# Performance work log

Hardware: AMD Instinct MI355X
Metric: run time of the kernel (lower is better)

## Reference

```python
import jax, jax.numpy as jnp
import numpy as np

N = 50000      # nodes
E = 800000     # edges
IN = 128       # in_dim
OUT = 128      # out_dim
R = 4          # num_relations
H = 8          # heads
D = OUT // H   # per-head dim
NEG_SLOPE = 0.2


def setup_inputs() -> dict:
    key = jax.random.key(0)
    ks = jax.random.split(key, 12)
    s = 0.05
    return {
        "node_inp": jax.random.normal(ks[0], (N, IN), dtype=jnp.float32),
        "edge_index": jax.random.randint(ks[1], (2, E), 0, N),
        "edge_type": jax.random.randint(ks[2], (E,), 0, R),
        # per-relation GATConv params
        "W_rel": jax.random.normal(ks[3], (R, IN, OUT), dtype=jnp.float32) * s,
        "att_src_rel": jax.random.normal(ks[4], (R, H, D), dtype=jnp.float32) * s,
        "att_dst_rel": jax.random.normal(ks[5], (R, H, D), dtype=jnp.float32) * s,
        "bias_rel": jax.random.normal(ks[6], (R, OUT), dtype=jnp.float32) * s,
        # linear layers
        "W_self": jax.random.normal(ks[7], (IN, OUT), dtype=jnp.float32) * s,   # lin_self
        "W_cross": jax.random.normal(ks[8], (OUT, OUT), dtype=jnp.float32) * s,  # lin_cross
        # lang_conv GAT params (lin_l is Bypass, so no weight matrix)
        "att_src_lang": jax.random.normal(ks[9], (H, D), dtype=jnp.float32) * s,
        "att_dst_lang": jax.random.normal(ks[10], (H, D), dtype=jnp.float32) * s,
        "bias_lang": jax.random.normal(ks[11], (OUT,), dtype=jnp.float32) * s,
    }


def _hgnn_forward(node_inp, edge_index, edge_type, W_rel, att_src_rel,
                  att_dst_rel, bias_rel, W_self, W_cross,
                  att_src_lang, att_dst_lang, bias_lang):
    src, dst = edge_index[0], edge_index[1]

    def rel_gat(W, a_s, a_d, b, mask):
        # standard PyG GATConv (single x, add_self_loops=False), restricted to
        # edges with this relation type via mask
        x = (node_inp @ W).reshape(N, H, D)                     # [N,H,D]
        es = jnp.einsum('nhd,hd->nh', x, a_s)
        ed = jnp.einsum('nhd,hd->nh', x, a_d)
        logit = jax.nn.leaky_relu(es[src] + ed[dst], NEG_SLOPE)  # [E,H]
        logit = jnp.where(mask[:, None], logit, -1e30)
        mx = jax.ops.segment_max(logit, dst, num_segments=N)     # [N,H]
        mx = jnp.maximum(mx, -1e30)                              # avoid -inf
        p = jnp.exp(logit - mx[dst]) * mask[:, None]
        den = jax.ops.segment_sum(p, dst, num_segments=N)        # [N,H]
        alpha = p / jnp.where(den > 0, den, 1.0)[dst]            # [E,H]
        msg = alpha[..., None] * x[src]                          # [E,H,D]
        out = jax.ops.segment_sum(msg, dst, num_segments=N)      # [N,H,D]
        tmask = jax.ops.segment_sum(mask.astype(jnp.float32), dst,
                                    num_segments=N) > 0          # [N] target nodes
        return out.reshape(N, OUT) + b, tmask

    rel_masks = edge_type[None, :] == jnp.arange(R)[:, None]     # [R,E]
    rel_out, tmask = jax.vmap(rel_gat)(W_rel, att_src_rel, att_dst_rel,
                                       bias_rel, rel_masks)      # [R,N,OUT],[R,N]
    h = jax.nn.gelu(rel_out, approximate=False) @ W_cross        # [R,N,OUT]

    S = node_inp @ W_self                                        # [N,OUT] self entries
    # lang_conv: per node i, GAT attention over entries {self(i)} U
    # {rel outputs at i for relations where i is a target}. lin_l = Bypass,
    # and since x is a single tensor in PyG, x_dst = rel_inputs[i] = S[i].
    ent = jnp.concatenate([S[None], h], axis=0).reshape(R + 1, N, H, D)
    valid = jnp.concatenate([jnp.ones((1, N), bool), tmask], axis=0)  # [R+1,N]
    ls = jnp.einsum('knhd,hd->knh', ent, att_src_lang)
    ld = jnp.einsum('nhd,hd->nh', ent[0], att_dst_lang)
    logit = jax.nn.leaky_relu(ls + ld[None], NEG_SLOPE)          # [R+1,N,H]
    logit = jnp.where(valid[..., None], logit, -jnp.inf)
    alpha = jax.nn.softmax(logit, axis=0)                        # self always valid
    out = jnp.einsum('knh,knhd->nhd', alpha, ent).reshape(N, OUT)
    return out + bias_lang


def reference(node_inp, edge_index, edge_type, W_rel, att_src_rel, att_dst_rel,
              bias_rel, W_self, W_cross, att_src_lang, att_dst_lang, bias_lang):
    return _hgnn_forward(node_inp, edge_index, edge_type, W_rel, att_src_rel,
                         att_dst_rel, bias_rel, W_self, W_cross,
                         att_src_lang, att_dst_lang, bias_lang)
```

## Files before the change

kernel.cpp:

```cpp
#include <hip/hip_runtime.h>
#include <hip/hip_bf16.h>
#include <math.h>

#define NN 50000
#define NE 800000
#define NREL 4
#define NHEAD 8
#define NSEG (NREL * NN)
#define BCAP 26

typedef __hip_bfloat16 bf16;
typedef short short8 __attribute__((ext_vector_type(8)));
typedef float floatx4 __attribute__((ext_vector_type(4)));

#define LOG2E 1.4426950408889634f

__device__ __forceinline__ float b2f(bf16 v) { return __bfloat162float(v); }
__device__ __forceinline__ float us2f(unsigned short u) {
    return __uint_as_float(((unsigned)u) << 16);
}
__device__ __forceinline__ unsigned short f2us(float v) {
    bf16 b = __float2bfloat16(v);
    return *(unsigned short*)&b;
}

__device__ __forceinline__ float gelu_f(float v) {
    float z = v * 0.70710678118654752f;
    float az = fabsf(z);
    float t = __builtin_amdgcn_rcpf(__builtin_fmaf(0.3275911f, az, 1.f));
    float p = t * (0.254829592f +
              t * (-0.284496736f +
              t * (1.421413741f +
              t * (-1.453152027f +
              t * 1.061405429f))));
    float ex = __builtin_amdgcn_exp2f(az * az * -LOG2E);
    float er = copysignf(1.f - p * ex, z);
    return 0.5f * v * (1.f + er);
}

__global__ void fill_kernel(float* __restrict__ out, int n) {
    int t = blockIdx.x * blockDim.x + threadIdx.x;
    if (t < n) out[t] = 1000.0f;
}

__global__ __launch_bounds__(256) void prep_scatter(
    const float* __restrict__ W_rel,
    const float* __restrict__ W_self,
    const float* __restrict__ W_cross,
    const float* __restrict__ a_src,
    const float* __restrict__ a_dst,
    const float* __restrict__ node_inp,
    const int* __restrict__ ei,
    const int* __restrict__ et,
    bf16* __restrict__ Wt, bf16* __restrict__ Wct,
    bf16* __restrict__ Ab,
    int* __restrict__ counts,
    unsigned short* __restrict__ bkt) {
    int t = blockIdx.x * blockDim.x + threadIdx.x;

    int src = 0, pos = BCAP;
    unsigned seg = 0;
    if (t < NE) {
        src = ei[t];
        int dst = ei[NE + t];
        seg = (unsigned)(et[t] * NN + dst);
        pos = atomicAdd(&counts[seg], 1);
    }

    if (t < 768 * 128) {
        int row = t >> 7, k = t & 127;
        float v;
        if (row < 512) {
            int r = row >> 7, c = row & 127;
            v = W_rel[(r * 128 + k) * 128 + c];
        } else if (row < 640) {
            v = W_self[k * 128 + (row - 512)];
        } else if (row < 704) {
            int q = row - 640;
            bool is_src = q < 32;
            int qq = is_src ? q : q - 32;
            int r = qq >> 3, h = qq & 7;
            const float* av = (is_src ? a_src : a_dst) + (r * 8 + h) * 16;
            const float* wr = W_rel + (size_t)(r * 128 + k) * 128 + h * 16;
            float s = 0.f;
            #pragma unroll
            for (int dd = 0; dd < 16; ++dd) s += wr[dd] * av[dd];
            v = s * LOG2E;
        } else {
            v = 0.f;
        }
        Wt[t] = __float2bfloat16(v);
    } else if (t < 768 * 128 + 128 * 128) {
        int u = t - 768 * 128;
        int n = u >> 7, k = u & 127;
        Wct[u] = __float2bfloat16(W_cross[k * 128 + n]);
    }

    if (t < NN * 16) {
        const float* ap = node_inp + (size_t)t * 8;
        float4 f0 = *(const float4*)ap;
        float4 f1 = *(const float4*)(ap + 4);
        short8 v = (short8){(short)f2us(f0.x), (short)f2us(f0.y),
                            (short)f2us(f0.z), (short)f2us(f0.w),
                            (short)f2us(f1.x), (short)f2us(f1.y),
                            (short)f2us(f1.z), (short)f2us(f1.w)};
        *(short8*)(Ab + (size_t)t * 8) = v;
    }

    if (t < NE && pos < BCAP)
        bkt[seg * (unsigned)BCAP + (unsigned)pos] = (unsigned short)src;
}

__global__ __launch_bounds__(256) void gemm_node(
    const bf16* __restrict__ Ab,
    const bf16* __restrict__ Bt,
    bf16* __restrict__ outb,
    float* __restrict__ outf,
    unsigned short* __restrict__ es_u,
    unsigned short* __restrict__ ed_u,
    int M)
{
    __shared__ __align__(16) char smem[25600];
    short (*As)[40] = (short (*)[40])smem;
    short (*Bs)[40] = (short (*)[40])(smem + 5120);

    const int tid  = threadIdx.x;
    const int wave = tid >> 6, lane = tid & 63;
    const int quad = lane >> 4, l16 = lane & 15;
    const int wr_ = wave & 1, wc = wave >> 1;
    const int row0 = blockIdx.x * 64;
    const int plane = blockIdx.y;
    const int col0 = plane * 256;

    floatx4 acc[2][8];
    #pragma unroll
    for (int i = 0; i < 2; ++i)
        #pragma unroll
        for (int j = 0; j < 8; ++j) acc[i][j] = (floatx4){0.f, 0.f, 0.f, 0.f};

    for (int k0 = 0; k0 < 128; k0 += 32) {
        {
            int c = tid;
            int r = c >> 2, off = (c & 3) * 8;
            int gr = row0 + r;
            short8 v = {0, 0, 0, 0, 0, 0, 0, 0};
            if (gr < M)
                v = *(const short8*)(Ab + (((size_t)gr) << 7) + k0 + off);
            *(short8*)&As[r][off] = v;
        }
        #pragma unroll
        for (int i = 0; i < 4; ++i) {
            int c = i * 256 + tid;
            int r = c >> 2, off = (c & 3) * 8;
            short8 w = *(const short8*)(Bt + (((size_t)(col0 + r)) << 7) + k0 + off);
            *(short8*)&Bs[r][off] = w;
        }
        __syncthreads();

        short8 av[2], bv[8];
        #pragma unroll
        for (int mt = 0; mt < 2; ++mt)
            av[mt] = *(const short8*)&As[wr_ * 32 + mt * 16 + l16][quad * 8];
        #pragma unroll
        for (int nt = 0; nt < 8; ++nt)
            bv[nt] = *(const short8*)&Bs[wc * 128 + nt * 16 + l16][quad * 8];
        #pragma unroll
        for (int mt = 0; mt < 2; ++mt)
            #pragma unroll
            for (int nt = 0; nt < 8; ++nt)
                acc[mt][nt] = __builtin_amdgcn_mfma_f32_16x16x32_bf16(
                    av[mt], bv[nt], acc[mt][nt], 0, 0, 0);
        __syncthreads();
    }

    const bool eswave = (plane == 2 && wc == 1);
    if (eswave) {
        #pragma unroll
        for (int mt = 0; mt < 2; ++mt) {
            #pragma unroll
            for (int reg = 0; reg < 4; ++reg) {
                int gr = row0 + wr_ * 32 + mt * 16 + quad * 4 + reg;
                if (gr >= M) continue;
                #pragma unroll
                for (int nt = 0; nt < 4; ++nt) {
                    int q = nt * 16 + l16;
                    unsigned short v = f2us(acc[mt][nt][reg]);
                    if (q < 32)
                        es_u[(unsigned)((q >> 3) * NN + gr) * 8u + (unsigned)(q & 7)] = v;
                    else
                        ed_u[(unsigned)(((q - 32) >> 3) * NN + gr) * 8u + (unsigned)((q - 32) & 7)] = v;
                }
            }
        }
    }

    float* ct = (float*)(smem + wave * 4352);
    const int rr2 = lane >> 2;
    const int cc0 = (lane & 3) * 16;

    for (int mt = 0; mt < 2; ++mt) {
        #pragma unroll
        for (int half = 0; half < 2; ++half) {
            if (!eswave) {
                #pragma unroll
                for (int nt = 0; nt < 4; ++nt)
                    #pragma unroll
                    for (int reg = 0; reg < 4; ++reg)
                        ct[(quad * 4 + reg) * 68 + nt * 16 + l16] =
                            acc[mt][half * 4 + nt][reg];
            }
            __syncthreads();
            if (!eswave) {
                int gr2 = row0 + wr_ * 32 + mt * 16 + rr2;
                if (gr2 < M) {
                    float4 f0 = *(const float4*)&ct[rr2 * 68 + cc0];
                    float4 f1 = *(const float4*)&ct[rr2 * 68 + cc0 + 4];
                    float4 f2 = *(const float4*)&ct[rr2 * 68 + cc0 + 8];
                    float4 f3 = *(const float4*)&ct[rr2 * 68 + cc0 + 12];
                    int lc = half * 64 + cc0;
                    if (plane == 2) {
                        float* dst = outf + (((size_t)gr2) << 7) + lc;
                        ((float4*)dst)[0] = f0;
                        ((float4*)dst)[1] = f1;
                        ((float4*)dst)[2] = f2;
                        ((float4*)dst)[3] = f3;
                    } else {
                        int rel = plane * 2 + wc;
                        float tmp[16] = {f0.x, f0.y, f0.z, f0.w, f1.x, f1.y, f1.z, f1.w,
                                         f2.x, f2.y, f2.z, f2.w, f3.x, f3.y, f3.z, f3.w};
                        short8 o0, o1;
                        #pragma unroll
                        for (int j = 0; j < 8; ++j) o0[j] = (short)f2us(tmp[j]);
                        #pragma unroll
                        for (int j = 0; j < 8; ++j) o1[j] = (short)f2us(tmp[8 + j]);
                        bf16* dst = outb + ((size_t)(rel * NN + gr2) << 7) + lc;
                        *(short8*)dst = o0;
                        *(short8*)(dst + 8) = o1;
                    }
                }
            }
            __syncthreads();
        }
    }
}

__global__ __launch_bounds__(256) void agg_kernel(
    const unsigned short* __restrict__ bkt, const int* __restrict__ counts,
    const bf16* __restrict__ Xb, const unsigned short* __restrict__ es_u,
    const unsigned short* __restrict__ ed_u, const float* __restrict__ bias_rel,
    bf16* __restrict__ Gb4, unsigned char* __restrict__ flag)
{
    const int rel = blockIdx.y;
    const int n = blockIdx.x * 4 + (threadIdx.x >> 6);
    if (n >= NN) return;
    const int l = threadIdx.x & 63;
    const int h = l >> 3;
    const int f = l * 2;
    const unsigned seg = (unsigned)(rel * NN + n);
    int cnt = __builtin_amdgcn_readfirstlane(counts[seg]);
    cnt = cnt < BCAP ? cnt : BCAP;
    const unsigned short* bk = bkt + seg * (unsigned)BCAP;
    const float edv = us2f(ed_u[seg * 8u + (unsigned)h]);
    float a0 = 0.f, a1 = 0.f, den = 0.f;
    const unsigned short* Xr = (const unsigned short*)Xb + (unsigned)rel * (unsigned)(NN * 128);
    const unsigned short* esr = es_u + (unsigned)rel * (unsigned)(NN * 8);

    int e = 0;
    for (; e + 3 < cnt; e += 4) {
        int s0 = __builtin_amdgcn_readfirstlane((int)bk[e]);
        int s1 = __builtin_amdgcn_readfirstlane((int)bk[e + 1]);
        int s2 = __builtin_amdgcn_readfirstlane((int)bk[e + 2]);
        int s3 = __builtin_amdgcn_readfirstlane((int)bk[e + 3]);
        float e0 = us2f(esr[(unsigned)s0 * 8u + (unsigned)h]);
        float e1 = us2f(esr[(unsigned)s1 * 8u + (unsigned)h]);
        float e2 = us2f(esr[(unsigned)s2 * 8u + (unsigned)h]);
        float e3 = us2f(esr[(unsigned)s3 * 8u + (unsigned)h]);
        ushort2 u0 = *(const ushort2*)(Xr + (unsigned)s0 * 128u + (unsigned)f);
        ushort2 u1 = *(const ushort2*)(Xr + (unsigned)s1 * 128u + (unsigned)f);
        ushort2 u2 = *(const ushort2*)(Xr + (unsigned)s2 * 128u + (unsigned)f);
        ushort2 u3 = *(const ushort2*)(Xr + (unsigned)s3 * 128u + (unsigned)f);
        float aa0 = e0 + edv, aa1 = e1 + edv, aa2 = e2 + edv, aa3 = e3 + edv;
        float w0 = __builtin_amdgcn_exp2f(fmaxf(aa0, 0.2f * aa0));
        float w1 = __builtin_amdgcn_exp2f(fmaxf(aa1, 0.2f * aa1));
        float w2 = __builtin_amdgcn_exp2f(fmaxf(aa2, 0.2f * aa2));
        float w3 = __builtin_amdgcn_exp2f(fmaxf(aa3, 0.2f * aa3));
        a0 += w0 * us2f(u0.x) + w1 * us2f(u1.x) + w2 * us2f(u2.x) + w3 * us2f(u3.x);
        a1 += w0 * us2f(u0.y) + w1 * us2f(u1.y) + w2 * us2f(u2.y) + w3 * us2f(u3.y);
        den += (w0 + w1) + (w2 + w3);
    }
    for (; e < cnt; ++e) {
        int s0 = __builtin_amdgcn_readfirstlane((int)bk[e]);
        float e0 = us2f(esr[(unsigned)s0 * 8u + (unsigned)h]);
        ushort2 u0 = *(const ushort2*)(Xr + (unsigned)s0 * 128u + (unsigned)f);
        float aa0 = e0 + edv;
        float w0 = __builtin_amdgcn_exp2f(fmaxf(aa0, 0.2f * aa0));
        a0 += w0 * us2f(u0.x);
        a1 += w0 * us2f(u0.y);
        den += w0;
    }

    float inv = den > 0.f ? __builtin_amdgcn_rcpf(den) : 0.f;
    float2 bv = *(const float2*)(bias_rel + (unsigned)rel * 128u + (unsigned)f);
    float v0 = gelu_f(__builtin_fmaf(a0, inv, bv.x));
    float v1 = gelu_f(__builtin_fmaf(a1, inv, bv.y));
    ushort2 o;
    o.x = f2us(v0);
    o.y = f2us(v1);
    *(ushort2*)((unsigned short*)Gb4 + ((unsigned)n * 4u + (unsigned)rel) * 128u + (unsigned)f) = o;
    if (l == 0) flag[(unsigned)n * 4u + (unsigned)rel] = (unsigned char)(cnt > 0);
}

__global__ __launch_bounds__(256) void gemm_lang(
    const bf16* __restrict__ A,
    const bf16* __restrict__ Bt,
    const unsigned char* __restrict__ flag,
    const float* __restrict__ asl_g,
    const float* __restrict__ adl_g,
    const float* __restrict__ bias_lang,
    float* __restrict__ out)
{
    __shared__ __align__(16) char smem[15360];
    short (*As)[40] = (short (*)[40])smem;
    short (*Bs)[40] = (short (*)[40])(smem + 5120);

    const int M = NN * NREL;
    const int tid  = threadIdx.x;
    const int wave = tid >> 6, lane = tid & 63;
    const int quad = lane >> 4, l16 = lane & 15;
    const int wr_ = wave & 1, wc = wave >> 1;
    const int row0 = blockIdx.x * 64;

    floatx4 acc[2][4];
    #pragma unroll
    for (int i = 0; i < 2; ++i)
        #pragma unroll
        for (int j = 0; j < 4; ++j) acc[i][j] = (floatx4){0.f, 0.f, 0.f, 0.f};

    for (int k0 = 0; k0 < 128; k0 += 32) {
        {
            int c = tid;
            int r = c >> 2, off = (c & 3) * 8;
            int gr = row0 + r;
            short8 v = {0, 0, 0, 0, 0, 0, 0, 0};
            if (gr < M)
                v = *(const short8*)(A + (((size_t)gr) << 7) + k0 + off);
            *(short8*)&As[r][off] = v;
        }
        #pragma unroll
        for (int i = 0; i < 2; ++i) {
            int c = tid * 2 + i;
            int r = c >> 2, off = (c & 3) * 8;
            short8 w = *(const short8*)(Bt + (((size_t)r) << 7) + k0 + off);
            *(short8*)&Bs[r][off] = w;
        }
        __syncthreads();

        short8 av[2], bv[4];
        #pragma unroll
        for (int mt = 0; mt < 2; ++mt)
            av[mt] = *(const short8*)&As[wr_ * 32 + mt * 16 + l16][quad * 8];
        #pragma unroll
        for (int nt = 0; nt < 4; ++nt)
            bv[nt] = *(const short8*)&Bs[wc * 64 + nt * 16 + l16][quad * 8];
        #pragma unroll
        for (int mt = 0; mt < 2; ++mt)
            #pragma unroll
            for (int nt = 0; nt < 4; ++nt)
                acc[mt][nt] = __builtin_amdgcn_mfma_f32_16x16x32_bf16(
                    av[mt], bv[nt], acc[mt][nt], 0, 0, 0);
        __syncthreads();
    }

    const int nb0 = blockIdx.x * 16 + wr_ * 8;
    #pragma unroll
    for (int nt = 0; nt < 4; ++nt) {
        int col = wc * 64 + nt * 16 + l16;
        float asl = asl_g[col];
        float adl = adl_g[col];
        float bl  = bias_lang[col];
        #pragma unroll
        for (int mt = 0; mt < 2; ++mt) {
            int node = nb0 + mt * 4 + quad;
            bool ok = node < NN;
            float Sv = ok ? out[(unsigned)node * 128u + (unsigned)col] : 0.f;
            float h0 = acc[mt][nt][0], h1 = acc[mt][nt][1];
            float h2 = acc[mt][nt][2], h3 = acc[mt][nt][3];
            float t0 = h0 * asl, t1 = h1 * asl, t2 = h2 * asl, t3 = h3 * asl;
            float ts = Sv * asl, td = Sv * adl;
            #pragma unroll
            for (int off = 1; off < 16; off <<= 1) {
                t0 += __shfl_xor(t0, off);
                t1 += __shfl_xor(t1, off);
                t2 += __shfl_xor(t2, off);
                t3 += __shfl_xor(t3, off);
                ts += __shfl_xor(ts, off);
                td += __shfl_xor(td, off);
            }
            unsigned fl = ok ? *(const unsigned*)(flag + (unsigned)node * 4u) : 0u;
            float aS = ts + td, a0 = t0 + td, a1 = t1 + td, a2 = t2 + td, a3 = t3 + td;
            float lS = fmaxf(aS, 0.2f * aS);
            float l0 = fmaxf(a0, 0.2f * a0);
            float l1 = fmaxf(a1, 0.2f * a1);
            float l2 = fmaxf(a2, 0.2f * a2);
            float l3 = fmaxf(a3, 0.2f * a3);
            bool v0 = (fl & 0x000000FFu) != 0, v1 = (fl & 0x0000FF00u) != 0;
            bool v2 = (fl & 0x00FF0000u) != 0, v3 = (fl & 0xFF000000u) != 0;
            float m = lS;
            if (v0) m = fmaxf(m, l0);
            if (v1) m = fmaxf(m, l1);
            if (v2) m = fmaxf(m, l2);
            if (v3) m = fmaxf(m, l3);
            float eS = __expf(lS - m);
            float e0 = v0 ? __expf(l0 - m) : 0.f;
            float e1 = v1 ? __expf(l1 - m) : 0.f;
            float e2 = v2 ? __expf(l2 - m) : 0.f;
            float e3 = v3 ? __expf(l3 - m) : 0.f;
            float sum = eS + e0 + e1 + e2 + e3;
            float o = eS * Sv + e0 * h0 + e1 * h1 + e2 * h2 + e3 * h3;
            o = o / sum + bl;
            if (ok) out[(unsigned)node * 128u + (unsigned)col] = o;
        }
    }
}

extern "C" void kernel_launch(void* const* d_in, const int* in_sizes, int n_in,
                              void* d_out, int out_size, void* d_ws, size_t ws_size,
                              hipStream_t stream) {
    const float* node_inp     = (const float*)d_in[0];
    const int*   edge_index   = (const int*)d_in[1];
    const int*   edge_type    = (const int*)d_in[2];
    const float* W_rel        = (const float*)d_in[3];
    const float* att_src_rel  = (const float*)d_in[4];
    const float* att_dst_rel  = (const float*)d_in[5];
    const float* bias_rel     = (const float*)d_in[6];
    const float* W_self       = (const float*)d_in[7];
    const float* W_cross      = (const float*)d_in[8];
    const float* att_src_lang = (const float*)d_in[9];
    const float* att_dst_lang = (const float*)d_in[10];
    const float* bias_lang    = (const float*)d_in[11];
    (void)in_sizes; (void)n_in;

    const size_t SZ_XB   = (size_t)NREL * NN * 128 * 2;
    const size_t SZ_ES   = (size_t)NREL * NN * 8 * 2;
    const size_t SZ_GB4  = (size_t)NREL * NN * 128 * 2;
    const size_t SZ_WT   = 768 * 128 * 2;
    const size_t SZ_WCT  = 128 * 128 * 2;
    const size_t SZ_BKT  = (size_t)NSEG * BCAP * 2;
    const size_t SZ_CNT  = (size_t)NSEG * 4;
    const size_t SZ_FLG  = (size_t)NN * 4;
    const size_t TOTAL = SZ_XB + 2 * SZ_ES + SZ_GB4 + SZ_WT + SZ_WCT +
                         SZ_BKT + SZ_CNT + SZ_FLG;

    if (ws_size < TOTAL) {
        fill_kernel<<<(out_size + 255) / 256, 256, 0, stream>>>((float*)d_out, out_size);
        return;
    }

    char* ws = (char*)d_ws;
    size_t o = 0;
    bf16*  Xb      = (bf16*)(ws + o);  o += SZ_XB;
    unsigned short* es_u = (unsigned short*)(ws + o); o += SZ_ES;
    unsigned short* ed_u = (unsigned short*)(ws + o); o += SZ_ES;
    bf16*  Gb4     = (bf16*)(ws + o);  o += SZ_GB4;
    bf16*  Wt      = (bf16*)(ws + o);  o += SZ_WT;
    bf16*  Wct     = (bf16*)(ws + o);  o += SZ_WCT;
    unsigned short* bkt = (unsigned short*)(ws + o); o += SZ_BKT;
    int*   counts  = (int*)(ws + o);   o += SZ_CNT;
    unsigned char* flag = (unsigned char*)(ws + o);
    float* S       = (float*)d_out;
    bf16*  Ab      = Gb4;

    hipMemsetAsync(counts, 0, SZ_CNT, stream);

    prep_scatter<<<(NE + 255) / 256, 256, 0, stream>>>(
        W_rel, W_self, W_cross, att_src_rel, att_dst_rel, node_inp,
        edge_index, edge_type, Wt, Wct, Ab, counts, bkt);

    dim3 g1((NN + 63) / 64, 3);
    gemm_node<<<g1, 256, 0, stream>>>(Ab, Wt, Xb, S, es_u, ed_u, NN);

    dim3 ga((NN + 3) / 4, NREL);
    agg_kernel<<<ga, 256, 0, stream>>>(bkt, counts, Xb, es_u, ed_u, bias_rel, Gb4, flag);

    dim3 g2((NREL * NN + 63) / 64, 1);
    gemm_lang<<<g2, 256, 0, stream>>>(Gb4, Wct, flag, att_src_lang, att_dst_lang,
                                      bias_lang, (float*)d_out);
}
```

Before: 289.8 us.

## Process four nodes per wave in aggregation with 16-byte gathers and nontemporal stores

The aggregation kernel now assigns 16 lanes per destination node, so each wave handles four nodes. Each lane gathers 8 bf16 features with one 16-byte load instead of 2 per lane, and edge indices are read in pairs. Nontemporal stores are added to the output writes in the node GEMM, the aggregation and the final lang GEMM to reduce cache pollution. Per-node edge counts now vary within a wave, which can cause divergence and loses the scalar readfirstlane indexing. The grid assumes NN divides evenly by 16 and the early bounds check is removed.

```diff
diff --git a/kernel.cpp b/kernel.cpp
--- a/kernel.cpp
+++ b/kernel.cpp
@@ -220,10 +220,10 @@
                     int lc = half * 64 + cc0;
                     if (plane == 2) {
                         float* dst = outf + (((size_t)gr2) << 7) + lc;
-                        ((float4*)dst)[0] = f0;
-                        ((float4*)dst)[1] = f1;
-                        ((float4*)dst)[2] = f2;
-                        ((float4*)dst)[3] = f3;
+                        __builtin_nontemporal_store(*(const floatx4*)&f0, (floatx4*)dst);
+                        __builtin_nontemporal_store(*(const floatx4*)&f1, (floatx4*)(dst + 4));
+                        __builtin_nontemporal_store(*(const floatx4*)&f2, (floatx4*)(dst + 8));
+                        __builtin_nontemporal_store(*(const floatx4*)&f3, (floatx4*)(dst + 12));
                     } else {
                         int rel = plane * 2 + wc;
                         float tmp[16] = {f0.x, f0.y, f0.z, f0.w, f1.x, f1.y, f1.z, f1.w,
@@ -250,64 +250,69 @@
     const unsigned short* __restrict__ ed_u, const float* __restrict__ bias_rel,
     bf16* __restrict__ Gb4, unsigned char* __restrict__ flag)
 {
-    const int rel = blockIdx.y;
-    const int n = blockIdx.x * 4 + (threadIdx.x >> 6);
-    if (n >= NN) return;
-    const int l = threadIdx.x & 63;
-    const int h = l >> 3;
-    const int f = l * 2;
+    const int rel  = blockIdx.y;
+    const int wave = threadIdx.x >> 6, l = threadIdx.x & 63;
+    const int n    = blockIdx.x * 16 + wave * 4 + (l >> 4);
+    const int l16  = l & 15;
+    const int f0   = l16 * 8;
+    const int h    = l16 >> 1;
+
     const unsigned seg = (unsigned)(rel * NN + n);
-    int cnt = __builtin_amdgcn_readfirstlane(counts[seg]);
+    int cnt = counts[seg];
     cnt = cnt < BCAP ? cnt : BCAP;
-    const unsigned short* bk = bkt + seg * (unsigned)BCAP;
+    const unsigned short* bk  = bkt + seg * (unsigned)BCAP;
     const float edv = us2f(ed_u[seg * 8u + (unsigned)h]);
-    float a0 = 0.f, a1 = 0.f, den = 0.f;
-    const unsigned short* Xr = (const unsigned short*)Xb + (unsigned)rel * (unsigned)(NN * 128);
+    const unsigned short* Xr  = (const unsigned short*)Xb +
+                                (size_t)rel * (size_t)(NN * 128);
     const unsigned short* esr = es_u + (unsigned)rel * (unsigned)(NN * 8);
 
+    float a[8];
+    #pragma unroll
+    for (int j = 0; j < 8; ++j) a[j] = 0.f;
+    float den = 0.f;
+
     int e = 0;
-    for (; e + 3 < cnt; e += 4) {
-        int s0 = __builtin_amdgcn_readfirstlane((int)bk[e]);
-        int s1 = __builtin_amdgcn_readfirstlane((int)bk[e + 1]);
-        int s2 = __builtin_amdgcn_readfirstlane((int)bk[e + 2]);
-        int s3 = __builtin_amdgcn_readfirstlane((int)bk[e + 3]);
+    for (; e + 1 < cnt; e += 2) {
+        unsigned pair = *(const unsigned*)(bk + e);
+        int s0 = (int)(pair & 0xFFFFu);
+        int s1 = (int)(pair >> 16);
         float e0 = us2f(esr[(unsigned)s0 * 8u + (unsigned)h]);
         float e1 = us2f(esr[(unsigned)s1 * 8u + (unsigned)h]);
-        float e2 = us2f(esr[(unsigned)s2 * 8u + (unsigned)h]);
-        float e3 = us2f(esr[(unsigned)s3 * 8u + (unsigned)h]);
-        ushort2 u0 = *(const ushort2*)(Xr + (unsigned)s0 * 128u + (unsigned)f);
-        ushort2 u1 = *(const ushort2*)(Xr + (unsigned)s1 * 128u + (unsigned)f);
-        ushort2 u2 = *(const ushort2*)(Xr + (unsigned)s2 * 128u + (unsigned)f);
-        ushort2 u3 = *(const ushort2*)(Xr + (unsigned)s3 * 128u + (unsigned)f);
-        float aa0 = e0 + edv, aa1 = e1 + edv, aa2 = e2 + edv, aa3 = e3 + edv;
+        short8 u0 = *(const short8*)(Xr + (size_t)s0 * 128 + f0);
+        short8 u1 = *(const short8*)(Xr + (size_t)s1 * 128 + f0);
+        float aa0 = e0 + edv, aa1 = e1 + edv;
         float w0 = __builtin_amdgcn_exp2f(fmaxf(aa0, 0.2f * aa0));
         float w1 = __builtin_amdgcn_exp2f(fmaxf(aa1, 0.2f * aa1));
-        float w2 = __builtin_amdgcn_exp2f(fmaxf(aa2, 0.2f * aa2));
-        float w3 = __builtin_amdgcn_exp2f(fmaxf(aa3, 0.2f * aa3));
-        a0 += w0 * us2f(u0.x) + w1 * us2f(u1.x) + w2 * us2f(u2.x) + w3 * us2f(u3.x);
-        a1 += w0 * us2f(u0.y) + w1 * us2f(u1.y) + w2 * us2f(u2.y) + w3 * us2f(u3.y);
-        den += (w0 + w1) + (w2 + w3);
-    }
-    for (; e < cnt; ++e) {
-        int s0 = __builtin_amdgcn_readfirstlane((int)bk[e]);
+        #pragma unroll
+        for (int j = 0; j < 8; ++j)
+            a[j] += w0 * us2f((unsigned short)u0[j]) +
+                    w1 * us2f((unsigned short)u1[j]);
+        den += w0 + w1;
+    }
+    if (e < cnt) {
+        int s0 = (int)bk[e];
         float e0 = us2f(esr[(unsigned)s0 * 8u + (unsigned)h]);
-        ushort2 u0 = *(const ushort2*)(Xr + (unsigned)s0 * 128u + (unsigned)f);
+        short8 u0 = *(const short8*)(Xr + (size_t)s0 * 128 + f0);
         float aa0 = e0 + edv;
         float w0 = __builtin_amdgcn_exp2f(fmaxf(aa0, 0.2f * aa0));
-        a0 += w0 * us2f(u0.x);
-        a1 += w0 * us2f(u0.y);
+        #pragma unroll
+        for (int j = 0; j < 8; ++j) a[j] += w0 * us2f((unsigned short)u0[j]);
         den += w0;
     }
 
     float inv = den > 0.f ? __builtin_amdgcn_rcpf(den) : 0.f;
-    float2 bv = *(const float2*)(bias_rel + (unsigned)rel * 128u + (unsigned)f);
-    float v0 = gelu_f(__builtin_fmaf(a0, inv, bv.x));
-    float v1 = gelu_f(__builtin_fmaf(a1, inv, bv.y));
-    ushort2 o;
-    o.x = f2us(v0);
-    o.y = f2us(v1);
-    *(ushort2*)((unsigned short*)Gb4 + ((unsigned)n * 4u + (unsigned)rel) * 128u + (unsigned)f) = o;
-    if (l == 0) flag[(unsigned)n * 4u + (unsigned)rel] = (unsigned char)(cnt > 0);
+    const float* bp = bias_rel + rel * 128 + f0;
+    float4 b0 = *(const float4*)bp;
+    float4 b1 = *(const float4*)(bp + 4);
+    float bb[8] = {b0.x, b0.y, b0.z, b0.w, b1.x, b1.y, b1.z, b1.w};
+    short8 o;
+    #pragma unroll
+    for (int j = 0; j < 8; ++j)
+        o[j] = (short)f2us(gelu_f(__builtin_fmaf(a[j], inv, bb[j])));
+    __builtin_nontemporal_store(o, (short8*)((unsigned short*)Gb4 +
+        ((size_t)((unsigned)n * 4u + (unsigned)rel)) * 128u + (unsigned)f0));
+    if (l16 == 0)
+        flag[(unsigned)n * 4u + (unsigned)rel] = (unsigned char)(cnt > 0);
 }
 
 __global__ __launch_bounds__(256) void gemm_lang(
@@ -418,7 +423,7 @@
             float sum = eS + e0 + e1 + e2 + e3;
             float o = eS * Sv + e0 * h0 + e1 * h1 + e2 * h2 + e3 * h3;
             o = o / sum + bl;
-            if (ok) out[(unsigned)node * 128u + (unsigned)col] = o;
+            if (ok) __builtin_nontemporal_store(o, &out[(unsigned)node * 128u + (unsigned)col]);
         }
     }
 }
@@ -479,7 +484,7 @@
     dim3 g1((NN + 63) / 64, 3);
     gemm_node<<<g1, 256, 0, stream>>>(Ab, Wt, Xb, S, es_u, ed_u, NN);
 
-    dim3 ga((NN + 3) / 4, NREL);
+    dim3 ga(NN / 16, NREL);
     agg_kernel<<<ga, 256, 0, stream>>>(bkt, counts, Xb, es_u, ed_u, bias_rel, Gb4, flag);
 
     dim3 g2((NREL * NN + 63) / 64, 1);
```

After: 282.6 us. -2.5%, faster.
